# Performance work log

Measured on AMD Instinct MI355X. Metric: run time of the kernel, lower is better.

## Reference

```python
import jax, jax.numpy as jnp
import numpy as np

B, T, TC, C, CC, H = 2, 2048, 512, 1024, 512, 16
D = C // H  # head dim = 64


def setup_inputs() -> dict:
    key = jax.random.key(0)
    ks = jax.random.split(key, 18)
    w = lambda k, i, o: (jax.random.normal(k, (i, o), jnp.float32) / np.sqrt(i).astype(np.float32))
    return {
        "x": jax.random.normal(ks[0], (B, T, C), jnp.float32),
        "cross_input": jax.random.normal(ks[1], (B, TC, CC), jnp.float32),
        "Wk": w(ks[2], C, C),  "bk": jnp.zeros((C,), jnp.float32),
        "Wq": w(ks[3], C, C),  "bq": jnp.zeros((C,), jnp.float32),
        "Wv": w(ks[4], C, C),  "bv": jnp.zeros((C,), jnp.float32),
        "Wck": w(ks[5], CC, C), "bck": jnp.zeros((C,), jnp.float32),
        "Wcq": w(ks[6], C, C),  "bcq": jnp.zeros((C,), jnp.float32),
        "Wcv": w(ks[7], CC, C), "bcv": jnp.zeros((C,), jnp.float32),
        "Wp": w(ks[8], C, C),   "bp": jnp.zeros((C,), jnp.float32),
    }


def _heads(t):
    # [B, L, C] -> [B, H, L, D]
    b, l, _ = t.shape
    return t.reshape(b, l, H, D).transpose(0, 2, 1, 3)


def reference(x, cross_input, Wk, bk, Wq, bq, Wv, bv, Wck, bck, Wcq, bcq, Wcv, bcv, Wp, bp):
    scale = np.float32(1.0 / np.sqrt(D))
    q = _heads(x @ Wq + bq)
    k = _heads(x @ Wk + bk)
    v = _heads(x @ Wv + bv)
    # causal self-attention with materialized scores (faithful to original)
    att = jnp.einsum("bhqd,bhkd->bhqk", q, k) * scale
    causal = jnp.tril(jnp.ones((T, T), bool))
    att = jnp.where(causal[None, None], att, -jnp.inf)
    y = jnp.einsum("bhqk,bhkd->bhqd", jax.nn.softmax(att, axis=-1), v)
    # cross-attention (no mask)
    qc = _heads(x @ Wcq + bcq)
    kc = _heads(cross_input @ Wck + bck)
    vc = _heads(cross_input @ Wcv + bcv)
    attc = jnp.einsum("bhqd,bhkd->bhqk", qc, kc) * scale
    y = y + jnp.einsum("bhqk,bhkd->bhqd", jax.nn.softmax(attc, axis=-1), vc)
    # merge heads + output projection (dropout prob = 0 -> identity)
    y = y.transpose(0, 2, 1, 3).reshape(x.shape[0], T, C)
    return y @ Wp + bp
```

## Files before the change

### kernel.cpp

```cpp
#include <hip/hip_runtime.h>
#include <hip/hip_bf16.h>
#include <type_traits>

typedef __bf16 bf16;
typedef __bf16 bf16x8 __attribute__((ext_vector_type(8)));
typedef float floatx4 __attribute__((ext_vector_type(4)));

#if __has_builtin(__builtin_amdgcn_exp2f)
#define EXP2(x) __builtin_amdgcn_exp2f(x)
#else
#define EXP2(x) exp2f(x)
#endif

__device__ __forceinline__ void glds16(const bf16* g, bf16* l) {
  __builtin_amdgcn_global_load_lds((const __attribute__((address_space(1))) void*)g,
                                   (__attribute__((address_space(3))) void*)l, 16, 0, 0);
}

__device__ __forceinline__ unsigned pack_bf16(float a, float b) {
  unsigned short ua = __builtin_bit_cast(unsigned short, (bf16)a);
  unsigned short ub = __builtin_bit_cast(unsigned short, (bf16)b);
  return (unsigned)ua | ((unsigned)ub << 16);
}

struct PrepArgs {
  const float* x; const float* xc;
  bf16* xbf; bf16* xcbf;
  const float* b4[4];
  const float* bc[2];
  float* bias4; float* biasc;
  const float* W[7];
  bf16* WT[7];
};

__global__ __launch_bounds__(256) void prep_kernel(PrepArgs a) {
  __shared__ bf16 tsh[32][33];
  const int bx = blockIdx.x, tid = threadIdx.x;
  if (bx < 4096) {
    int i = bx * 256 + tid;
    float4 f = ((const float4*)a.x)[i];
    bf16 t[4] = {(bf16)f.x, (bf16)f.y, (bf16)f.z, (bf16)f.w};
    *(uint2*)&a.xbf[(long)i * 4] = *(const uint2*)t;
  } else if (bx < 4608) {
    int i = (bx - 4096) * 256 + tid;
    float4 f = ((const float4*)a.xc)[i];
    bf16 t[4] = {(bf16)f.x, (bf16)f.y, (bf16)f.z, (bf16)f.w};
    *(uint2*)&a.xcbf[(long)i * 4] = *(const uint2*)t;
  } else if (bx < 4632) {
    int lb = bx - 4608;
    if (lb < 16) { int i = lb * 256 + tid; a.bias4[i] = a.b4[i >> 10][i & 1023]; }
    else         { int i = (lb - 16) * 256 + tid; a.biasc[i] = a.bc[i >> 10][i & 1023]; }
  } else {
    int t = bx - 4632, w, R, bxw, byw;
    if (t < 5120) { w = t >> 10; R = 1024; int l = t & 1023; bxw = l & 31; byw = l >> 5; }
    else { int t2 = t - 5120; w = 5 + (t2 >> 9); R = 512; int l = t2 & 511; bxw = l & 31; byw = l >> 5; }
    const float* in = a.W[w];
    bf16* out = a.WT[w];
    int tx = tid & 31, ty = tid >> 5;
    int c = bxw * 32 + tx;
#pragma unroll
    for (int i = 0; i < 4; i++) {
      int r = byw * 32 + ty + i * 8;
      tsh[ty + i * 8][tx] = (bf16)in[(long)r * 1024 + c];
    }
    __syncthreads();
    int oc = byw * 32 + tx;
#pragma unroll
    for (int i = 0; i < 4; i++) {
      int orr = bxw * 32 + ty + i * 8;
      out[(long)orr * R + oc] = tsh[tx][ty + i * 8];
    }
  }
}

template <typename OutT>
__global__ __launch_bounds__(256, 3) void gemm128(const bf16* __restrict__ A,
                                                  const bf16* __restrict__ Bt,
                                                  const float* __restrict__ bias,
                                                  OutT* __restrict__ C,
                                                  int M, int N, int K, int ldc,
                                                  bf16* __restrict__ Vt,
                                                  int vcol0, int vcol1, int Lt, int tok_shift) {
  __shared__ alignas(16) bf16 As[128 * 32];
  __shared__ alignas(16) bf16 Bs[128 * 32];
  const int tid = threadIdx.x, wave = tid >> 6, lane = tid & 63;
  const int l16 = lane & 15, l4 = lane >> 4;
  const int wm = wave & 1, wn = wave >> 1;
  const int n0 = blockIdx.x * 128, m0 = blockIdx.y * 128;
  const int lrow = lane >> 2, lch = (lane & 3) * 8;

  floatx4 acc[4][4];
#pragma unroll
  for (int mt = 0; mt < 4; mt++)
#pragma unroll
    for (int nt = 0; nt < 4; nt++) acc[mt][nt] = (floatx4){0.f, 0.f, 0.f, 0.f};

  const bf16* Ag = A + (long)(m0 + wave * 32 + lrow) * K + lch;
  const bf16* Bg = Bt + (long)(n0 + wave * 32 + lrow) * K + lch;
  bf16* Al = &As[(wave * 32) * 32];
  bf16* Bl = &Bs[(wave * 32) * 32];

  for (int k0 = 0; k0 < K; k0 += 32) {
    __syncthreads();
    glds16(Ag + k0, Al);
    glds16(Ag + k0 + (long)16 * K, Al + 16 * 32);
    glds16(Bg + k0, Bl);
    glds16(Bg + k0 + (long)16 * K, Bl + 16 * 32);
    __syncthreads();
    bf16x8 a[4], b[4];
#pragma unroll
    for (int mt = 0; mt < 4; mt++) a[mt] = *(const bf16x8*)&As[(wm * 64 + mt * 16 + l16) * 32 + l4 * 8];
#pragma unroll
    for (int nt = 0; nt < 4; nt++) b[nt] = *(const bf16x8*)&Bs[(wn * 64 + nt * 16 + l16) * 32 + l4 * 8];
#pragma unroll
    for (int mt = 0; mt < 4; mt++)
#pragma unroll
      for (int nt = 0; nt < 4; nt++)
        acc[mt][nt] = __builtin_amdgcn_mfma_f32_16x16x32_bf16(a[mt], b[nt], acc[mt][nt], 0, 0, 0);
  }

  const bool vpath = (vcol0 >= 0) && (n0 >= vcol0) && (n0 < vcol1);
  if (!vpath) {
    const int coladj = (vcol0 >= 0 && n0 >= vcol1) ? (vcol1 - vcol0) : 0;
#pragma unroll
    for (int nt = 0; nt < 4; nt++) {
      int col = n0 + wn * 64 + nt * 16 + l16;
      float bv = bias[col];
#pragma unroll
      for (int mt = 0; mt < 4; mt++)
#pragma unroll
        for (int r = 0; r < 4; r++) {
          int row = m0 + wm * 64 + mt * 16 + l4 * 4 + r;
          float v = acc[mt][nt][r] + bv;
          if constexpr (std::is_same_v<OutT, float>) C[(long)row * ldc + col - coladj] = v;
          else                                       C[(long)row * ldc + col - coladj] = (bf16)v;
        }
    }
  } else {
#pragma unroll
    for (int nt = 0; nt < 4; nt++) {
      int col = n0 + wn * 64 + nt * 16 + l16;
      int c = col - vcol0, hh = c >> 6, dd = c & 63;
      float bv = bias[col];
#pragma unroll
      for (int mt = 0; mt < 4; mt++) {
        int t0 = m0 + wm * 64 + mt * 16 + l4 * 4;
        int bb = t0 >> tok_shift, t = t0 & ((1 << tok_shift) - 1);
        bf16 tmp[4];
#pragma unroll
        for (int r = 0; r < 4; r++) tmp[r] = (bf16)(acc[mt][nt][r] + bv);
        *(uint2*)&Vt[(((long)bb * 16 + hh) * 64 + dd) * Lt + t] = *(const uint2*)tmp;
      }
    }
  }
}

__global__ __launch_bounds__(256, 2) void attn_kernel(const bf16* __restrict__ QKQc,
                                                      const bf16* __restrict__ VtB,
                                                      const bf16* __restrict__ KcB,
                                                      const bf16* __restrict__ VctB,
                                                      bf16* __restrict__ Y) {
  __shared__ float2 Mbuf[4][4][16];
  __shared__ alignas(16) bf16 U[4 * 64 * 72];
  const int tid = threadIdx.x, w = tid >> 6, lane = tid & 63;
  const int l16 = lane & 15, l4 = lane >> 4;
  const int bh = blockIdx.x, h = bh & 15, b = bh >> 4;
  const int qt = 31 - (int)blockIdx.y;
  const int q0 = qt * 64;
  const int wk = w * 32;
  bf16* Pw = U + w * (64 * 48);
  const float NEG = -1e30f;

  float o_self[16];

  for (int phase = 0; phase < 2; phase++) {
    const bf16 *Qb, *Kb, *Vtb;
    int kstr, vtstr, nkt;
    if (phase == 0) {
      Qb = QKQc + (long)b * 2048 * 3072 + h * 64;
      Kb = Qb + 1024;                              kstr = 3072;
      Vtb = VtB + ((long)b * 16 + h) * 64 * 2048;  vtstr = 2048;
      nkt = (qt + 2) >> 1;
    } else {
      Qb = QKQc + (long)b * 2048 * 3072 + h * 64 + 2048;
      Kb = KcB + (long)b * 512 * 1024 + h * 64;    kstr = 1024;
      Vtb = VctB + ((long)b * 16 + h) * 64 * 512;  vtstr = 512;
      nkt = 4;
    }

    __syncthreads();

    bf16x8 qf[4][2];
#pragma unroll
    for (int qtt = 0; qtt < 4; qtt++) {
      const bf16* qp = Qb + (long)(q0 + qtt * 16 + l16) * 3072 + l4 * 8;
#pragma unroll
      for (int ds = 0; ds < 2; ds++) {
        bf16x8 v = *(const bf16x8*)(qp + ds * 32);
#pragma unroll
        for (int j = 0; j < 8; j++) v[j] = (bf16)((float)v[j] * 0.18033688f);
        qf[qtt][ds] = v;
      }
    }

    float m_i[4], l_i[4];
#pragma unroll
    for (int qtt = 0; qtt < 4; qtt++) { m_i[qtt] = NEG; l_i[qtt] = 0.f; }
    floatx4 oacc[4][4];
#pragma unroll
    for (int mtd = 0; mtd < 4; mtd++)
#pragma unroll
      for (int qtt = 0; qtt < 4; qtt++) oacc[mtd][qtt] = (floatx4){0.f, 0.f, 0.f, 0.f};

    bf16x8 kc[2][2], kn[2][2];
#pragma unroll
    for (int mt = 0; mt < 2; mt++)
#pragma unroll
      for (int ds = 0; ds < 2; ds++)
        kc[mt][ds] = *(const bf16x8*)(Kb + (long)(wk + mt * 16 + l16) * kstr + ds * 32 + l4 * 8);

    for (int kt = 0; kt < nkt; kt++) {
      const int kbase = kt * 128 + wk;
      bf16x8 vc[4];
#pragma unroll
      for (int mtd = 0; mtd < 4; mtd++)
        vc[mtd] = *(const bf16x8*)(Vtb + (long)(mtd * 16 + l16) * vtstr + kbase + l4 * 8);

      floatx4 sacc[2][4];
#pragma unroll
      for (int mt = 0; mt < 2; mt++)
#pragma unroll
        for (int qtt = 0; qtt < 4; qtt++) sacc[mt][qtt] = (floatx4){0.f, 0.f, 0.f, 0.f};
#pragma unroll
      for (int ds = 0; ds < 2; ds++)
#pragma unroll
        for (int mt = 0; mt < 2; mt++)
#pragma unroll
          for (int qtt = 0; qtt < 4; qtt++)
            sacc[mt][qtt] = __builtin_amdgcn_mfma_f32_16x16x32_bf16(kc[mt][ds], qf[qtt][ds], sacc[mt][qtt], 0, 0, 0);

      if (kt + 1 < nkt) {
        const int nb = kbase + 128;
#pragma unroll
        for (int mt = 0; mt < 2; mt++)
#pragma unroll
          for (int ds = 0; ds < 2; ds++)
            kn[mt][ds] = *(const bf16x8*)(Kb + (long)(nb + mt * 16 + l16) * kstr + ds * 32 + l4 * 8);
      }

      if (phase == 0 && kt == nkt - 1) {
#pragma unroll
        for (int mt = 0; mt < 2; mt++) {
          int keyb = kbase + mt * 16 + l4 * 4;
#pragma unroll
          for (int qtt = 0; qtt < 4; qtt++) {
            int q = q0 + qtt * 16 + l16;
#pragma unroll
            for (int r = 0; r < 4; r++)
              if (keyb + r > q) sacc[mt][qtt][r] = NEG;
          }
        }
      }

      float alpha[4];
      unsigned pd[4][2][2];
      int changed = 0;
#pragma unroll
      for (int qtt = 0; qtt < 4; qtt++) {
        float mx = fmaxf(fmaxf(fmaxf(sacc[0][qtt][0], sacc[0][qtt][1]), fmaxf(sacc[0][qtt][2], sacc[0][qtt][3])),
                         fmaxf(fmaxf(sacc[1][qtt][0], sacc[1][qtt][1]), fmaxf(sacc[1][qtt][2], sacc[1][qtt][3])));
        mx = fmaxf(mx, __shfl_xor(mx, 16));
        mx = fmaxf(mx, __shfl_xor(mx, 32));
        mx = fmaxf(mx, m_i[qtt]);
        alpha[qtt] = EXP2(m_i[qtt] - mx);
        changed |= (mx > m_i[qtt]) ? 1 : 0;
        m_i[qtt] = mx;
        float rs = 0.f;
#pragma unroll
        for (int mt = 0; mt < 2; mt++) {
          float p0 = EXP2(sacc[mt][qtt][0] - mx), p1 = EXP2(sacc[mt][qtt][1] - mx);
          float p2 = EXP2(sacc[mt][qtt][2] - mx), p3 = EXP2(sacc[mt][qtt][3] - mx);
          rs += (p0 + p1) + (p2 + p3);
          pd[qtt][mt][0] = pack_bf16(p0, p1);
          pd[qtt][mt][1] = pack_bf16(p2, p3);
        }
        rs += __shfl_xor(rs, 16);
        rs += __shfl_xor(rs, 32);
        l_i[qtt] = l_i[qtt] * alpha[qtt] + rs;
      }
      if (__any(changed)) {
#pragma unroll
        for (int mtd = 0; mtd < 4; mtd++)
#pragma unroll
          for (int qtt = 0; qtt < 4; qtt++)
#pragma unroll
            for (int r = 0; r < 4; r++) oacc[mtd][qtt][r] *= alpha[qtt];
      }

#pragma unroll
      for (int qtt = 0; qtt < 4; qtt++)
#pragma unroll
        for (int mt = 0; mt < 2; mt++) {
          uint2 u = {pd[qtt][mt][0], pd[qtt][mt][1]};
          *(uint2*)&Pw[(qtt * 16 + l16) * 48 + mt * 16 + l4 * 4] = u;
        }
#pragma unroll
      for (int qtt = 0; qtt < 4; qtt++) {
        bf16x8 pf = *(const bf16x8*)&Pw[(qtt * 16 + l16) * 48 + l4 * 8];
#pragma unroll
        for (int mtd = 0; mtd < 4; mtd++)
          oacc[mtd][qtt] = __builtin_amdgcn_mfma_f32_16x16x32_bf16(vc[mtd], pf, oacc[mtd][qtt], 0, 0, 0);
      }
#pragma unroll
      for (int mt = 0; mt < 2; mt++)
#pragma unroll
        for (int ds = 0; ds < 2; ds++) kc[mt][ds] = kn[mt][ds];
    }

    if (l4 == 0) {
#pragma unroll
      for (int qtt = 0; qtt < 4; qtt++) Mbuf[w][qtt][l16] = make_float2(m_i[qtt], l_i[qtt]);
    }
    __syncthreads();
    float myscale[4], denom[4];
#pragma unroll
    for (int qtt = 0; qtt < 4; qtt++) {
      float2 s0 = Mbuf[0][qtt][l16], s1 = Mbuf[1][qtt][l16];
      float2 s2 = Mbuf[2][qtt][l16], s3 = Mbuf[3][qtt][l16];
      float M = fmaxf(fmaxf(s0.x, s1.x), fmaxf(s2.x, s3.x));
      denom[qtt] = EXP2(s0.x - M) * s0.y + EXP2(s1.x - M) * s1.y +
                   EXP2(s2.x - M) * s2.y + EXP2(s3.x - M) * s3.y;
      myscale[qtt] = EXP2(m_i[qtt] - M);
    }
#pragma unroll
    for (int qtt = 0; qtt < 4; qtt++)
#pragma unroll
      for (int mtd = 0; mtd < 4; mtd++) {
        float s = myscale[qtt];
        uint2 u = {pack_bf16(oacc[mtd][qtt][0] * s, oacc[mtd][qtt][1] * s),
                   pack_bf16(oacc[mtd][qtt][2] * s, oacc[mtd][qtt][3] * s)};
        *(uint2*)&U[((w * 64) + qtt * 16 + l16) * 72 + mtd * 16 + l4 * 4] = u;
      }
    __syncthreads();
    float sum[16];
#pragma unroll
    for (int j = 0; j < 16; j++) sum[j] = 0.f;
#pragma unroll
    for (int s = 0; s < 4; s++) {
      bf16x8 c0 = *(const bf16x8*)&U[((s * 64) + w * 16 + l16) * 72 + l4 * 16];
      bf16x8 c1 = *(const bf16x8*)&U[((s * 64) + w * 16 + l16) * 72 + l4 * 16 + 8];
#pragma unroll
      for (int j = 0; j < 8; j++) { sum[j] += (float)c0[j]; sum[8 + j] += (float)c1[j]; }
    }
    float invd = 1.0f / denom[w];
    if (phase == 0) {
#pragma unroll
      for (int j = 0; j < 16; j++) o_self[j] = sum[j] * invd;
    } else {
      long row = (long)b * 2048 + q0 + w * 16 + l16;
      bf16 out[16];
#pragma unroll
      for (int j = 0; j < 16; j++) out[j] = (bf16)(o_self[j] + sum[j] * invd);
      *(bf16x8*)&Y[row * 1024 + h * 64 + l4 * 16] = *(const bf16x8*)&out[0];
      *(bf16x8*)&Y[row * 1024 + h * 64 + l4 * 16 + 8] = *(const bf16x8*)&out[8];
    }
  }
}

extern "C" void kernel_launch(void* const* d_in, const int* in_sizes, int n_in,
                              void* d_out, int out_size, void* d_ws, size_t ws_size,
                              hipStream_t stream) {
  const float* x   = (const float*)d_in[0];
  const float* xc  = (const float*)d_in[1];
  const float* Wk  = (const float*)d_in[2];  const float* bk  = (const float*)d_in[3];
  const float* Wq  = (const float*)d_in[4];  const float* bq  = (const float*)d_in[5];
  const float* Wv  = (const float*)d_in[6];  const float* bv  = (const float*)d_in[7];
  const float* Wck = (const float*)d_in[8];  const float* bck = (const float*)d_in[9];
  const float* Wcq = (const float*)d_in[10]; const float* bcq = (const float*)d_in[11];
  const float* Wcv = (const float*)d_in[12]; const float* bcv = (const float*)d_in[13];
  const float* Wp  = (const float*)d_in[14]; const float* bp  = (const float*)d_in[15];

  char* ws = (char*)d_ws;
  const size_t MB = 1ull << 20;
  bf16*  WT_all = (bf16*)(ws + 0);
  bf16*  WC_all = (bf16*)(ws + 8 * MB);
  bf16*  WpT    = (bf16*)(ws + 10 * MB);
  bf16*  xbf    = (bf16*)(ws + 12 * MB);
  bf16*  Yb     = xbf;
  bf16*  xcbf   = (bf16*)(ws + 20 * MB);
  float* bias4  = (float*)(ws + 21 * MB);
  float* biasc  = (float*)(ws + 21 * MB + 65536);
  bf16*  QKQc   = (bf16*)(ws + 22 * MB);
  bf16*  VtB    = (bf16*)(ws + 46 * MB);
  bf16*  KcB    = (bf16*)(ws + 54 * MB);
  bf16*  VctB   = (bf16*)(ws + 56 * MB);

  PrepArgs pa;
  pa.x = x; pa.xc = xc; pa.xbf = xbf; pa.xcbf = xcbf;
  pa.b4[0] = bq; pa.b4[1] = bk; pa.b4[2] = bv; pa.b4[3] = bcq;
  pa.bc[0] = bck; pa.bc[1] = bcv;
  pa.bias4 = bias4; pa.biasc = biasc;
  pa.W[0] = Wq;  pa.WT[0] = WT_all + 0ll * 1024 * 1024;
  pa.W[1] = Wk;  pa.WT[1] = WT_all + 1ll * 1024 * 1024;
  pa.W[2] = Wv;  pa.WT[2] = WT_all + 2ll * 1024 * 1024;
  pa.W[3] = Wcq; pa.WT[3] = WT_all + 3ll * 1024 * 1024;
  pa.W[4] = Wp;  pa.WT[4] = WpT;
  pa.W[5] = Wck; pa.WT[5] = WC_all + 0ll * 1024 * 512;
  pa.W[6] = Wcv; pa.WT[6] = WC_all + 1ll * 1024 * 512;
  prep_kernel<<<10776, 256, 0, stream>>>(pa);

  gemm128<bf16><<<dim3(32, 32), 256, 0, stream>>>(xbf, WT_all, bias4, QKQc,
                                                  4096, 4096, 1024, 3072,
                                                  VtB, 2048, 3072, 2048, 11);
  gemm128<bf16><<<dim3(16, 8), 256, 0, stream>>>(xcbf, WC_all, biasc, KcB,
                                                 1024, 2048, 512, 1024,
                                                 VctB, 1024, 2048, 512, 9);

  attn_kernel<<<dim3(32, 32), 256, 0, stream>>>(QKQc, VtB, KcB, VctB, Yb);

  gemm128<float><<<dim3(8, 32), 256, 0, stream>>>(Yb, WpT, bp, (float*)d_out,
                                                  4096, 1024, 1024, 1024,
                                                  nullptr, -1, -1, 0, 0);
}
```

Before: 261.4 us.

## Keep P in registers via permuted V layout, lazy rescale, fold scale into weights

Writes the transposed V with a permuted token order so the softmax P fragment produced by the QK MFMA can feed the PV MFMA directly from registers, removing the per-tile LDS write/read of P. The online-softmax max is only updated when it grows by more than 8 (log2 domain), which skips most accumulator rescales. The Q scale factor is folded into the Wq/Wcq weights and biases during prep, so the per-load multiply in the attention kernel goes away. The lazy max update allows exponents up to 2^8 before rescaling, a small overflow/precision risk in bf16 P values.

```diff
diff --git a/kernel.cpp b/kernel.cpp
--- a/kernel.cpp
+++ b/kernel.cpp
@@ -5,6 +5,7 @@
 typedef __bf16 bf16;
 typedef __bf16 bf16x8 __attribute__((ext_vector_type(8)));
 typedef float floatx4 __attribute__((ext_vector_type(4)));
+typedef unsigned int uint32x4 __attribute__((ext_vector_type(4)));
 
 #if __has_builtin(__builtin_amdgcn_exp2f)
 #define EXP2(x) __builtin_amdgcn_exp2f(x)
@@ -48,20 +49,29 @@
     *(uint2*)&a.xcbf[(long)i * 4] = *(const uint2*)t;
   } else if (bx < 4632) {
     int lb = bx - 4608;
-    if (lb < 16) { int i = lb * 256 + tid; a.bias4[i] = a.b4[i >> 10][i & 1023]; }
-    else         { int i = (lb - 16) * 256 + tid; a.biasc[i] = a.bc[i >> 10][i & 1023]; }
+    if (lb < 16) {
+      int i = lb * 256 + tid;
+      int sec = i >> 10;
+      float v = a.b4[sec][i & 1023];
+      if (sec == 0 || sec == 3) v *= 0.18033688f;
+      a.bias4[i] = v;
+    } else {
+      int i = (lb - 16) * 256 + tid;
+      a.biasc[i] = a.bc[i >> 10][i & 1023];
+    }
   } else {
     int t = bx - 4632, w, R, bxw, byw;
     if (t < 5120) { w = t >> 10; R = 1024; int l = t & 1023; bxw = l & 31; byw = l >> 5; }
     else { int t2 = t - 5120; w = 5 + (t2 >> 9); R = 512; int l = t2 & 511; bxw = l & 31; byw = l >> 5; }
     const float* in = a.W[w];
     bf16* out = a.WT[w];
+    const float sc = (w == 0 || w == 3) ? 0.18033688f : 1.0f;
     int tx = tid & 31, ty = tid >> 5;
     int c = bxw * 32 + tx;
 #pragma unroll
     for (int i = 0; i < 4; i++) {
       int r = byw * 32 + ty + i * 8;
-      tsh[ty + i * 8][tx] = (bf16)in[(long)r * 1024 + c];
+      tsh[ty + i * 8][tx] = (bf16)(in[(long)r * 1024 + c] * sc);
     }
     __syncthreads();
     int oc = byw * 32 + tx;
@@ -146,6 +156,7 @@
       for (int mt = 0; mt < 4; mt++) {
         int t0 = m0 + wm * 64 + mt * 16 + l4 * 4;
         int bb = t0 >> tok_shift, t = t0 & ((1 << tok_shift) - 1);
+        t = (t & ~31) | (((t >> 2) & 3) << 3) | (((t >> 4) & 1) << 2) | (t & 3);
         bf16 tmp[4];
 #pragma unroll
         for (int r = 0; r < 4; r++) tmp[r] = (bf16)(acc[mt][nt][r] + bv);
@@ -168,7 +179,6 @@
   const int qt = 31 - (int)blockIdx.y;
   const int q0 = qt * 64;
   const int wk = w * 32;
-  bf16* Pw = U + w * (64 * 48);
   const float NEG = -1e30f;
 
   float o_self[16];
@@ -195,12 +205,7 @@
     for (int qtt = 0; qtt < 4; qtt++) {
       const bf16* qp = Qb + (long)(q0 + qtt * 16 + l16) * 3072 + l4 * 8;
 #pragma unroll
-      for (int ds = 0; ds < 2; ds++) {
-        bf16x8 v = *(const bf16x8*)(qp + ds * 32);
-#pragma unroll
-        for (int j = 0; j < 8; j++) v[j] = (bf16)((float)v[j] * 0.18033688f);
-        qf[qtt][ds] = v;
-      }
+      for (int ds = 0; ds < 2; ds++) qf[qtt][ds] = *(const bf16x8*)(qp + ds * 32);
     }
 
     float m_i[4], l_i[4];
@@ -262,55 +267,39 @@
         }
       }
 
-      float alpha[4];
-      unsigned pd[4][2][2];
-      int changed = 0;
 #pragma unroll
       for (int qtt = 0; qtt < 4; qtt++) {
         float mx = fmaxf(fmaxf(fmaxf(sacc[0][qtt][0], sacc[0][qtt][1]), fmaxf(sacc[0][qtt][2], sacc[0][qtt][3])),
                          fmaxf(fmaxf(sacc[1][qtt][0], sacc[1][qtt][1]), fmaxf(sacc[1][qtt][2], sacc[1][qtt][3])));
         mx = fmaxf(mx, __shfl_xor(mx, 16));
         mx = fmaxf(mx, __shfl_xor(mx, 32));
-        mx = fmaxf(mx, m_i[qtt]);
-        alpha[qtt] = EXP2(m_i[qtt] - mx);
-        changed |= (mx > m_i[qtt]) ? 1 : 0;
-        m_i[qtt] = mx;
-        float rs = 0.f;
-#pragma unroll
-        for (int mt = 0; mt < 2; mt++) {
-          float p0 = EXP2(sacc[mt][qtt][0] - mx), p1 = EXP2(sacc[mt][qtt][1] - mx);
-          float p2 = EXP2(sacc[mt][qtt][2] - mx), p3 = EXP2(sacc[mt][qtt][3] - mx);
-          rs += (p0 + p1) + (p2 + p3);
-          pd[qtt][mt][0] = pack_bf16(p0, p1);
-          pd[qtt][mt][1] = pack_bf16(p2, p3);
-        }
+        float mold = m_i[qtt];
+        float nm = fmaxf(mx, mold);
+        bool upd = nm > mold + 8.f;
+        float al = upd ? EXP2(mold - nm) : 1.f;
+        float mcur = upd ? nm : mold;
+        m_i[qtt] = mcur;
+        float p0 = EXP2(sacc[0][qtt][0] - mcur), p1 = EXP2(sacc[0][qtt][1] - mcur);
+        float p2 = EXP2(sacc[0][qtt][2] - mcur), p3 = EXP2(sacc[0][qtt][3] - mcur);
+        float p4 = EXP2(sacc[1][qtt][0] - mcur), p5 = EXP2(sacc[1][qtt][1] - mcur);
+        float p6 = EXP2(sacc[1][qtt][2] - mcur), p7 = EXP2(sacc[1][qtt][3] - mcur);
+        float rs = ((p0 + p1) + (p2 + p3)) + ((p4 + p5) + (p6 + p7));
         rs += __shfl_xor(rs, 16);
         rs += __shfl_xor(rs, 32);
-        l_i[qtt] = l_i[qtt] * alpha[qtt] + rs;
-      }
-      if (__any(changed)) {
-#pragma unroll
-        for (int mtd = 0; mtd < 4; mtd++)
-#pragma unroll
-          for (int qtt = 0; qtt < 4; qtt++)
-#pragma unroll
-            for (int r = 0; r < 4; r++) oacc[mtd][qtt][r] *= alpha[qtt];
-      }
-
-#pragma unroll
-      for (int qtt = 0; qtt < 4; qtt++)
-#pragma unroll
-        for (int mt = 0; mt < 2; mt++) {
-          uint2 u = {pd[qtt][mt][0], pd[qtt][mt][1]};
-          *(uint2*)&Pw[(qtt * 16 + l16) * 48 + mt * 16 + l4 * 4] = u;
+        l_i[qtt] = l_i[qtt] * al + rs;
+        if (__any((int)upd)) {
+#pragma unroll
+          for (int mtd = 0; mtd < 4; mtd++)
+#pragma unroll
+            for (int r = 0; r < 4; r++) oacc[mtd][qtt][r] *= al;
         }
-#pragma unroll
-      for (int qtt = 0; qtt < 4; qtt++) {
-        bf16x8 pf = *(const bf16x8*)&Pw[(qtt * 16 + l16) * 48 + l4 * 8];
+        uint32x4 pu = {pack_bf16(p0, p1), pack_bf16(p2, p3), pack_bf16(p4, p5), pack_bf16(p6, p7)};
+        bf16x8 pf = __builtin_bit_cast(bf16x8, pu);
 #pragma unroll
         for (int mtd = 0; mtd < 4; mtd++)
           oacc[mtd][qtt] = __builtin_amdgcn_mfma_f32_16x16x32_bf16(vc[mtd], pf, oacc[mtd][qtt], 0, 0, 0);
       }
+
 #pragma unroll
       for (int mt = 0; mt < 2; mt++)
 #pragma unroll
```

New measurement: 261.7 us. No clear change (+0.1%).
